# Kernel optimization log

Hardware: AMD Instinct MI355X
Metric: run time of the kernel (lower is better)

Reference implementation:

```python
import jax, jax.numpy as jnp
import numpy as np

B, S, DIM = 32, 1, 4096
N_HEADS, N_KV, HD = 32, 8, 128
N_REP = N_HEADS // N_KV
MAX_SEQ = 2048


def _rope(x, cos, sin):
    # x: [b, s, h, d]; cos/sin: [s, d//2]; rotate consecutive pairs
    x2 = x.reshape(*x.shape[:-1], HD // 2, 2)
    x0, x1 = x2[..., 0], x2[..., 1]
    c = cos[None, :, None, :]
    s = sin[None, :, None, :]
    o0 = x0 * c - x1 * s
    o1 = x0 * s + x1 * c
    return jnp.stack([o0, o1], axis=-1).reshape(x.shape)


def setup_inputs() -> dict:
    key = jax.random.key(0)
    ks = jax.random.split(key, 9)
    start_pos = 2047
    # true RoPE frequencies at position start_pos
    inv_freq = 1.0 / (10000.0 ** (np.arange(0, HD, 2, dtype=np.float32) / HD))
    ang = (start_pos * inv_freq).astype(np.float32)[None, :]  # [1, HD//2]
    return {
        "x": jax.random.normal(ks[0], (B, S, DIM), jnp.float32),
        "freqs_cos": jnp.asarray(np.cos(ang)),
        "freqs_sin": jnp.asarray(np.sin(ang)),
        "wq": jax.random.normal(ks[1], (DIM, DIM), jnp.float32) * 0.02,
        "wk": jax.random.normal(ks[2], (N_KV * HD, DIM), jnp.float32) * 0.02,
        "wv": jax.random.normal(ks[3], (N_KV * HD, DIM), jnp.float32) * 0.02,
        "wo": jax.random.normal(ks[4], (DIM, DIM), jnp.float32) * 0.02,
        "cache_k": jax.random.normal(ks[5], (B, MAX_SEQ, N_KV, HD), jnp.float32),
        "cache_v": jax.random.normal(ks[6], (B, MAX_SEQ, N_KV, HD), jnp.float32),
        "start_pos": start_pos,
    }


def reference(x, freqs_cos, freqs_sin, wq, wk, wv, wo, cache_k, cache_v, start_pos):
    b, s, dim = x.shape  # s == 1 (decode)
    xq = (x @ wq.T).reshape(b, s, N_HEADS, HD)
    xk = (x @ wk.T).reshape(b, s, N_KV, HD)
    xv = (x @ wv.T).reshape(b, s, N_KV, HD)
    xq = _rope(xq, freqs_cos, freqs_sin)
    xk = _rope(xk, freqs_cos, freqs_sin)
    # KV-cache scatter write at start_pos
    cache_k = jax.lax.dynamic_update_slice(cache_k, xk, (0, start_pos, 0, 0))
    cache_v = jax.lax.dynamic_update_slice(cache_v, xv, (0, start_pos, 0, 0))
    t = start_pos + s
    keys = cache_k[:, :t]    # [b, t, kv, hd]
    values = cache_v[:, :t]  # [b, t, kv, hd]
    # GQA: group query heads over kv heads (no repeat_kv materialization)
    q = xq[:, 0].reshape(b, N_KV, N_REP, HD)  # [b, kv, rep, hd]
    scale = HD ** -0.5
    attn = jnp.einsum("bkrd,btkd->bkrt", q, keys) * scale  # [b, kv, rep, t]
    attn = jax.nn.softmax(attn.astype(jnp.float32), axis=-1).astype(q.dtype)
    out = jnp.einsum("bkrt,btkd->bkrd", attn, values).reshape(b, s, dim)
    return out @ wo.T
```

## Files before the change

### kernel.cpp

```cpp
#include <hip/hip_runtime.h>
#include <math.h>

#define B_ 32
#define DIM_ 4096
#define NKV_ 8
#define HD_ 128
#define T_ 2048
#define KS_ 16
#define QKV_ROWS_ 6144
#define O_ROWS_ 4096

#define Q_OFF    0
#define KNEW_OFF (Q_OFF + B_*DIM_)
#define VNEW_OFF (KNEW_OFF + B_*NKV_*HD_)
#define AO_OFF   (VNEW_OFF + B_*NKV_*HD_)
#define PQKV_OFF (AO_OFF + B_*DIM_)
#define PO_OFF   (PQKV_OFF + KS_*QKV_ROWS_*B_)

__device__ __forceinline__ void fma4(float4& a, const float4& x, float w) {
    a.x = fmaf(x.x, w, a.x); a.y = fmaf(x.y, w, a.y);
    a.z = fmaf(x.z, w, a.z); a.w = fmaf(x.w, w, a.w);
}

template<int NROWS>
__global__ __launch_bounds__(256) void gemm_split(
    const float* __restrict__ X, const float* __restrict__ W0,
    const float* __restrict__ W1, const float* __restrict__ W2,
    float* __restrict__ part)
{
    __shared__ float xs[32][36];
    __shared__ float wsh[32][132];
    const int rb = blockIdx.x, ks = blockIdx.y;
    const int row0 = rb * 128;
    const float* W; int wr0;
    if (NROWS == 4096 || row0 < 4096) { W = W0; wr0 = row0; }
    else if (row0 < 5120)             { W = W1; wr0 = row0 - 4096; }
    else                              { W = W2; wr0 = row0 - 5120; }
    const int tid = threadIdx.x;
    const int rt = tid & 31, bt = tid >> 5;
    float4 acc[4];
    acc[0] = acc[1] = acc[2] = acc[3] = make_float4(0.f,0.f,0.f,0.f);
    const int kc0 = ks * 256;
    const int xb = tid >> 3, xkq = tid & 7;
    for (int kt = 0; kt < 8; ++kt) {
        const int kc = kc0 + kt * 32;
        __syncthreads();
        {
            float4 v = *(const float4*)(X + xb * DIM_ + kc + xkq * 4);
            xs[xkq*4+0][xb] = v.x; xs[xkq*4+1][xb] = v.y;
            xs[xkq*4+2][xb] = v.z; xs[xkq*4+3][xb] = v.w;
        }
        #pragma unroll
        for (int j = 0; j < 4; ++j) {
            int f = tid + 256 * j;
            int r = f >> 3, kq = f & 7;
            float4 v = *(const float4*)(W + (wr0 + r) * DIM_ + kc + kq * 4);
            wsh[kq*4+0][r] = v.x; wsh[kq*4+1][r] = v.y;
            wsh[kq*4+2][r] = v.z; wsh[kq*4+3][r] = v.w;
        }
        __syncthreads();
        #pragma unroll
        for (int k = 0; k < 32; ++k) {
            float4 xv = *(const float4*)&xs[k][bt*4];
            float4 wv = *(const float4*)&wsh[k][rt*4];
            fma4(acc[0], xv, wv.x);
            fma4(acc[1], xv, wv.y);
            fma4(acc[2], xv, wv.z);
            fma4(acc[3], xv, wv.w);
        }
    }
    #pragma unroll
    for (int j = 0; j < 4; ++j) {
        const int row = row0 + rt * 4 + j;
        *(float4*)(part + (ks * NROWS + row) * 32 + bt * 4) = acc[j];
    }
}

__global__ __launch_bounds__(256) void reduce_rope(
    const float* __restrict__ part, const float* __restrict__ fc,
    const float* __restrict__ fs, float* __restrict__ qout,
    float* __restrict__ kout, float* __restrict__ vout)
{
    const int t = blockIdx.x * 256 + threadIdx.x;
    const int b = t & 31;
    const int row0 = (t >> 5) * 2;
    float s0 = 0.f, s1 = 0.f;
    #pragma unroll
    for (int ks = 0; ks < KS_; ++ks) {
        const float* p = part + (ks * QKV_ROWS_ + row0) * 32 + b;
        s0 += p[0];
        s1 += p[32];
    }
    if (row0 < 5120) {
        const int i = (row0 & 127) >> 1;
        const float c = fc[i], s = fs[i];
        const float o0 = s0 * c - s1 * s;
        const float o1 = s0 * s + s1 * c;
        if (row0 < 4096) {
            qout[b * 4096 + row0]     = o0;
            qout[b * 4096 + row0 + 1] = o1;
        } else {
            const int lr = row0 - 4096;
            kout[b * 1024 + lr]     = o0;
            kout[b * 1024 + lr + 1] = o1;
        }
    } else {
        const int lr = row0 - 5120;
        vout[b * 1024 + lr]     = s0;
        vout[b * 1024 + lr + 1] = s1;
    }
}

__global__ __launch_bounds__(512) void attn_decode(
    const float* __restrict__ q, const float* __restrict__ knew,
    const float* __restrict__ vnew, const float* __restrict__ ck,
    const float* __restrict__ cv, float* __restrict__ ao)
{
    __shared__ float sc[4 * 2052];
    __shared__ float red[16];
    __shared__ float red3[2048];
    const int b  = blockIdx.x >> 3;
    const int kv = blockIdx.x & 7;
    const int tid = threadIdx.x;
    const int w  = tid >> 6;
    const int ln = tid & 63;
    const int r  = ln >> 4;
    const int ds = ln & 15;
    const float scale = 0.08838834764831845f;

    const float* qp = q + b * 4096 + (kv * 4 + r) * 128 + ds * 8;
    const float4 qa = *(const float4*)qp;
    const float4 qb = *(const float4*)(qp + 4);
    const float* ckb = ck + ((b * 2048) * 8 + kv) * 128;
    const float* knb = knew + (b * 8 + kv) * 128 + ds * 8;

    for (int i = 0; i < 32; ++i) {
        const int tbase = w + 64 * i;
        float4 ka[8], kb[8];
        #pragma unroll
        for (int u = 0; u < 8; ++u) {
            const int t = tbase + 8 * u;
            const float* kp = (t == 2047) ? knb : (ckb + t * 1024 + ds * 8);
            ka[u] = *(const float4*)kp;
            kb[u] = *(const float4*)(kp + 4);
        }
        #pragma unroll
        for (int u = 0; u < 8; ++u) {
            const int t = tbase + 8 * u;
            float d = ka[u].x*qa.x + ka[u].y*qa.y + ka[u].z*qa.z + ka[u].w*qa.w
                    + kb[u].x*qb.x + kb[u].y*qb.y + kb[u].z*qb.z + kb[u].w*qb.w;
            d += __shfl_xor(d, 1);
            d += __shfl_xor(d, 2);
            d += __shfl_xor(d, 4);
            d += __shfl_xor(d, 8);
            if (ds == 0) sc[r * 2052 + t] = d * scale;
        }
    }
    __syncthreads();

    const int m128 = tid & 127;
    const int r2 = tid >> 7;
    float mloc = -1e30f;
    #pragma unroll
    for (int j = 0; j < 16; ++j)
        mloc = fmaxf(mloc, sc[r2 * 2052 + m128 + j * 128]);
    #pragma unroll
    for (int o = 1; o < 64; o <<= 1)
        mloc = fmaxf(mloc, __shfl_xor(mloc, o));
    if (ln == 0) red[w] = mloc;
    __syncthreads();
    const float m = fmaxf(red[r2 * 2], red[r2 * 2 + 1]);
    float sloc = 0.f;
    #pragma unroll
    for (int j = 0; j < 16; ++j) {
        const int idx = r2 * 2052 + m128 + j * 128;
        const float p = __expf(sc[idx] - m);
        sc[idx] = p;
        sloc += p;
    }
    #pragma unroll
    for (int o = 1; o < 64; o <<= 1)
        sloc += __shfl_xor(sloc, o);
    if (ln == 0) red[8 + w] = sloc;
    __syncthreads();

    const int tp = tid >> 7;
    const int r3 = (tid >> 5) & 3;
    const int dq = tid & 31;
    const float* cvb = cv + ((b * 2048) * 8 + kv) * 128 + dq * 4;
    const float* vnb = vnew + (b * 8 + kv) * 128 + dq * 4;
    float4 acc[4];
    acc[0] = acc[1] = acc[2] = acc[3] = make_float4(0.f,0.f,0.f,0.f);
    for (int j = 0; j < 512; j += 4) {
        #pragma unroll
        for (int u = 0; u < 4; ++u) {
            const int t = tp + 4 * (j + u);
            const float* vp = (t == 2047) ? vnb : (cvb + t * 1024);
            const float4 v = *(const float4*)vp;
            const float p = sc[r3 * 2052 + t];
            fma4(acc[u], v, p);
        }
    }
    float4 asum;
    asum.x = (acc[0].x + acc[1].x) + (acc[2].x + acc[3].x);
    asum.y = (acc[0].y + acc[1].y) + (acc[2].y + acc[3].y);
    asum.z = (acc[0].z + acc[1].z) + (acc[2].z + acc[3].z);
    asum.w = (acc[0].w + acc[1].w) + (acc[2].w + acc[3].w);
    *(float4*)&red3[((tp * 4 + r3) * 32 + dq) * 4] = asum;
    __syncthreads();
    if (tid < 128) {
        const int rr = tid >> 5, dqq = tid & 31;
        float4 s = make_float4(0.f,0.f,0.f,0.f);
        #pragma unroll
        for (int t4 = 0; t4 < 4; ++t4) {
            const float4 v = *(const float4*)&red3[((t4 * 4 + rr) * 32 + dqq) * 4];
            s.x += v.x; s.y += v.y; s.z += v.z; s.w += v.w;
        }
        const float invl = 1.f / (red[8 + rr * 2] + red[8 + rr * 2 + 1]);
        s.x *= invl; s.y *= invl; s.z *= invl; s.w *= invl;
        *(float4*)(ao + b * 4096 + (kv * 4 + rr) * 128 + dqq * 4) = s;
    }
}

__global__ __launch_bounds__(256) void reduce_out(
    const float* __restrict__ part, float* __restrict__ out)
{
    const int t = blockIdx.x * 256 + threadIdx.x;
    const int b = t & 31, row = t >> 5;
    float s = 0.f;
    #pragma unroll
    for (int ks = 0; ks < KS_; ++ks)
        s += part[(ks * O_ROWS_ + row) * 32 + b];
    out[b * 4096 + row] = s;
}

extern "C" void kernel_launch(void* const* d_in, const int* in_sizes, int n_in,
                              void* d_out, int out_size, void* d_ws, size_t ws_size,
                              hipStream_t stream)
{
    const float* x  = (const float*)d_in[0];
    const float* fc = (const float*)d_in[1];
    const float* fs = (const float*)d_in[2];
    const float* wq = (const float*)d_in[3];
    const float* wk = (const float*)d_in[4];
    const float* wv = (const float*)d_in[5];
    const float* wo = (const float*)d_in[6];
    const float* ck = (const float*)d_in[7];
    const float* cv = (const float*)d_in[8];
    float* ws   = (float*)d_ws;
    float* q    = ws + Q_OFF;
    float* knew = ws + KNEW_OFF;
    float* vnew = ws + VNEW_OFF;
    float* ao   = ws + AO_OFF;
    float* pqkv = ws + PQKV_OFF;
    float* po   = ws + PO_OFF;

    gemm_split<QKV_ROWS_><<<dim3(48, 16), 256, 0, stream>>>(x, wq, wk, wv, pqkv);
    reduce_rope<<<384, 256, 0, stream>>>(pqkv, fc, fs, q, knew, vnew);
    attn_decode<<<256, 512, 0, stream>>>(q, knew, vnew, ck, cv, ao);
    gemm_split<O_ROWS_><<<dim3(32, 16), 256, 0, stream>>>(ao, wo, wo, wo, po);
    reduce_out<<<512, 256, 0, stream>>>(po, (float*)d_out);
}
```

Baseline: 647.1 us.

## Split decode attention over sequence chunks with flash-decoding merge kernel

Replaces the single attention kernel (256 blocks, one per batch and KV head) with a split-K variant that gives each block a 512-token chunk, for 1024 blocks. Each block also reuses one K load across all four query heads of the group. A new merge kernel combines the per-chunk partial outputs using the saved max and sum values. The aim is more parallelism across the GPU to saturate bandwidth on the 128 MB KV cache read, at the cost of an extra launch and some partial-result traffic.

```diff
diff --git a/kernel.cpp b/kernel.cpp
--- a/kernel.cpp
+++ b/kernel.cpp
@@ -9,6 +9,7 @@
 #define KS_ 16
 #define QKV_ROWS_ 6144
 #define O_ROWS_ 4096
+#define NSPLIT_ 4
 
 #define Q_OFF    0
 #define KNEW_OFF (Q_OFF + B_*DIM_)
@@ -16,6 +17,8 @@
 #define AO_OFF   (VNEW_OFF + B_*NKV_*HD_)
 #define PQKV_OFF (AO_OFF + B_*DIM_)
 #define PO_OFF   (PQKV_OFF + KS_*QKV_ROWS_*B_)
+#define OPART_OFF (PO_OFF + KS_*O_ROWS_*B_)
+#define ML_OFF   (OPART_OFF + B_*NKV_*NSPLIT_*4*HD_)
 
 __device__ __forceinline__ void fma4(float4& a, const float4& x, float w) {
     a.x = fmaf(x.x, w, a.x); a.y = fmaf(x.y, w, a.y);
@@ -111,115 +114,168 @@
     }
 }
 
-__global__ __launch_bounds__(512) void attn_decode(
+__global__ __launch_bounds__(256, 4) void attn_split(
     const float* __restrict__ q, const float* __restrict__ knew,
     const float* __restrict__ vnew, const float* __restrict__ ck,
-    const float* __restrict__ cv, float* __restrict__ ao)
-{
-    __shared__ float sc[4 * 2052];
-    __shared__ float red[16];
-    __shared__ float red3[2048];
-    const int b  = blockIdx.x >> 3;
-    const int kv = blockIdx.x & 7;
+    const float* __restrict__ cv, float* __restrict__ opart,
+    float* __restrict__ ml)
+{
+    __shared__ float sct[512 * 4];
+    __shared__ float red[2048];
+    const int sp = blockIdx.x & 3;
+    const int kv = (blockIdx.x >> 2) & 7;
+    const int b  = blockIdx.x >> 5;
     const int tid = threadIdx.x;
     const int w  = tid >> 6;
     const int ln = tid & 63;
-    const int r  = ln >> 4;
-    const int ds = ln & 15;
+    const int t0 = sp * 512;
     const float scale = 0.08838834764831845f;
 
-    const float* qp = q + b * 4096 + (kv * 4 + r) * 128 + ds * 8;
-    const float4 qa = *(const float4*)qp;
-    const float4 qb = *(const float4*)(qp + 4);
-    const float* ckb = ck + ((b * 2048) * 8 + kv) * 128;
-    const float* knb = knew + (b * 8 + kv) * 128 + ds * 8;
-
-    for (int i = 0; i < 32; ++i) {
-        const int tbase = w + 64 * i;
-        float4 ka[8], kb[8];
+    const int tl = ln >> 4, dsl = ln & 15;
+    float4 qr[4][2];
+    #pragma unroll
+    for (int r = 0; r < 4; ++r) {
+        const float* qp = q + b * 4096 + (kv * 4 + r) * 128 + dsl * 8;
+        qr[r][0] = *(const float4*)qp;
+        qr[r][1] = *(const float4*)(qp + 4);
+    }
+    const float* ckb = ck + ((size_t)(b * 2048) * 8 + kv) * 128;
+    const float* knb = knew + (b * 8 + kv) * 128 + dsl * 8;
+
+    for (int tt = 0; tt < 32; tt += 4) {
+        float4 ka[4][2];
+        int ri[4];
+        #pragma unroll
+        for (int u = 0; u < 4; ++u) {
+            ri[u] = w * 128 + (tt + u) * 4 + tl;
+            const int gt = t0 + ri[u];
+            const float* kp = (gt == 2047) ? knb
+                              : (ckb + (size_t)gt * 1024 + dsl * 8);
+            ka[u][0] = *(const float4*)kp;
+            ka[u][1] = *(const float4*)(kp + 4);
+        }
+        #pragma unroll
+        for (int u = 0; u < 4; ++u) {
+            float d[4];
+            #pragma unroll
+            for (int r = 0; r < 4; ++r) {
+                float t1 = ka[u][0].x*qr[r][0].x + ka[u][0].y*qr[r][0].y
+                         + ka[u][0].z*qr[r][0].z + ka[u][0].w*qr[r][0].w;
+                float t2 = ka[u][1].x*qr[r][1].x + ka[u][1].y*qr[r][1].y
+                         + ka[u][1].z*qr[r][1].z + ka[u][1].w*qr[r][1].w;
+                float dd = t1 + t2;
+                dd += __shfl_xor(dd, 1);
+                dd += __shfl_xor(dd, 2);
+                dd += __shfl_xor(dd, 4);
+                dd += __shfl_xor(dd, 8);
+                d[r] = dd * scale;
+            }
+            if (dsl == 0)
+                *(float4*)&sct[ri[u] * 4] = make_float4(d[0], d[1], d[2], d[3]);
+        }
+    }
+    __syncthreads();
+
+    float vals[8];
+    #pragma unroll
+    for (int j = 0; j < 8; ++j)
+        vals[j] = sct[(j * 64 + ln) * 4 + w];
+    float m = vals[0];
+    #pragma unroll
+    for (int j = 1; j < 8; ++j) m = fmaxf(m, vals[j]);
+    #pragma unroll
+    for (int o = 1; o < 64; o <<= 1)
+        m = fmaxf(m, __shfl_xor(m, o));
+    float l = 0.f;
+    #pragma unroll
+    for (int j = 0; j < 8; ++j) {
+        const float p = __expf(vals[j] - m);
+        sct[(j * 64 + ln) * 4 + w] = p;
+        l += p;
+    }
+    #pragma unroll
+    for (int o = 1; o < 64; o <<= 1)
+        l += __shfl_xor(l, o);
+    if (ln == 0) {
+        const int idx = ((b * 8 + kv) * 4 + sp) * 8 + w * 2;
+        ml[idx]     = m;
+        ml[idx + 1] = l;
+    }
+    __syncthreads();
+
+    float2 acc[4];
+    #pragma unroll
+    for (int r = 0; r < 4; ++r) acc[r] = make_float2(0.f, 0.f);
+    const float* cvb = cv + ((size_t)(b * 2048) * 8 + kv) * 128 + ln * 2;
+    const float* vnb = vnew + (b * 8 + kv) * 128 + ln * 2;
+    for (int j = 0; j < 128; j += 8) {
+        float2 vv[8];
         #pragma unroll
         for (int u = 0; u < 8; ++u) {
-            const int t = tbase + 8 * u;
-            const float* kp = (t == 2047) ? knb : (ckb + t * 1024 + ds * 8);
-            ka[u] = *(const float4*)kp;
-            kb[u] = *(const float4*)(kp + 4);
+            const int gt = t0 + w * 128 + j + u;
+            const float* vp = (gt == 2047) ? vnb : (cvb + (size_t)gt * 1024);
+            vv[u] = *(const float2*)vp;
         }
         #pragma unroll
         for (int u = 0; u < 8; ++u) {
-            const int t = tbase + 8 * u;
-            float d = ka[u].x*qa.x + ka[u].y*qa.y + ka[u].z*qa.z + ka[u].w*qa.w
-                    + kb[u].x*qb.x + kb[u].y*qb.y + kb[u].z*qb.z + kb[u].w*qb.w;
-            d += __shfl_xor(d, 1);
-            d += __shfl_xor(d, 2);
-            d += __shfl_xor(d, 4);
-            d += __shfl_xor(d, 8);
-            if (ds == 0) sc[r * 2052 + t] = d * scale;
-        }
-    }
+            const int ri = w * 128 + j + u;
+            const float4 p4 = *(const float4*)&sct[ri * 4];
+            acc[0].x = fmaf(vv[u].x, p4.x, acc[0].x);
+            acc[0].y = fmaf(vv[u].y, p4.x, acc[0].y);
+            acc[1].x = fmaf(vv[u].x, p4.y, acc[1].x);
+            acc[1].y = fmaf(vv[u].y, p4.y, acc[1].y);
+            acc[2].x = fmaf(vv[u].x, p4.z, acc[2].x);
+            acc[2].y = fmaf(vv[u].y, p4.z, acc[2].y);
+            acc[3].x = fmaf(vv[u].x, p4.w, acc[3].x);
+            acc[3].y = fmaf(vv[u].y, p4.w, acc[3].y);
+        }
+    }
+    #pragma unroll
+    for (int r = 0; r < 4; ++r)
+        *(float2*)&red[((w * 4 + r) * 64 + ln) * 2] = acc[r];
     __syncthreads();
-
-    const int m128 = tid & 127;
-    const int r2 = tid >> 7;
-    float mloc = -1e30f;
-    #pragma unroll
-    for (int j = 0; j < 16; ++j)
-        mloc = fmaxf(mloc, sc[r2 * 2052 + m128 + j * 128]);
-    #pragma unroll
-    for (int o = 1; o < 64; o <<= 1)
-        mloc = fmaxf(mloc, __shfl_xor(mloc, o));
-    if (ln == 0) red[w] = mloc;
-    __syncthreads();
-    const float m = fmaxf(red[r2 * 2], red[r2 * 2 + 1]);
-    float sloc = 0.f;
-    #pragma unroll
-    for (int j = 0; j < 16; ++j) {
-        const int idx = r2 * 2052 + m128 + j * 128;
-        const float p = __expf(sc[idx] - m);
-        sc[idx] = p;
-        sloc += p;
-    }
-    #pragma unroll
-    for (int o = 1; o < 64; o <<= 1)
-        sloc += __shfl_xor(sloc, o);
-    if (ln == 0) red[8 + w] = sloc;
-    __syncthreads();
-
-    const int tp = tid >> 7;
-    const int r3 = (tid >> 5) & 3;
-    const int dq = tid & 31;
-    const float* cvb = cv + ((b * 2048) * 8 + kv) * 128 + dq * 4;
-    const float* vnb = vnew + (b * 8 + kv) * 128 + dq * 4;
-    float4 acc[4];
-    acc[0] = acc[1] = acc[2] = acc[3] = make_float4(0.f,0.f,0.f,0.f);
-    for (int j = 0; j < 512; j += 4) {
-        #pragma unroll
-        for (int u = 0; u < 4; ++u) {
-            const int t = tp + 4 * (j + u);
-            const float* vp = (t == 2047) ? vnb : (cvb + t * 1024);
-            const float4 v = *(const float4*)vp;
-            const float p = sc[r3 * 2052 + t];
-            fma4(acc[u], v, p);
-        }
-    }
-    float4 asum;
-    asum.x = (acc[0].x + acc[1].x) + (acc[2].x + acc[3].x);
-    asum.y = (acc[0].y + acc[1].y) + (acc[2].y + acc[3].y);
-    asum.z = (acc[0].z + acc[1].z) + (acc[2].z + acc[3].z);
-    asum.w = (acc[0].w + acc[1].w) + (acc[2].w + acc[3].w);
-    *(float4*)&red3[((tp * 4 + r3) * 32 + dq) * 4] = asum;
-    __syncthreads();
-    if (tid < 128) {
-        const int rr = tid >> 5, dqq = tid & 31;
-        float4 s = make_float4(0.f,0.f,0.f,0.f);
-        #pragma unroll
-        for (int t4 = 0; t4 < 4; ++t4) {
-            const float4 v = *(const float4*)&red3[((t4 * 4 + rr) * 32 + dqq) * 4];
-            s.x += v.x; s.y += v.y; s.z += v.z; s.w += v.w;
-        }
-        const float invl = 1.f / (red[8 + rr * 2] + red[8 + rr * 2 + 1]);
-        s.x *= invl; s.y *= invl; s.z *= invl; s.w *= invl;
-        *(float4*)(ao + b * 4096 + (kv * 4 + rr) * 128 + dqq * 4) = s;
-    }
+    {
+        const int r = tid >> 6, dd = tid & 63;
+        float2 s = make_float2(0.f, 0.f);
+        #pragma unroll
+        for (int ww = 0; ww < 4; ++ww) {
+            const float2 v = *(const float2*)&red[((ww * 4 + r) * 64 + dd) * 2];
+            s.x += v.x; s.y += v.y;
+        }
+        const int ob = (((b * 8 + kv) * 4 + sp) * 4 + r) * 128 + dd * 2;
+        *(float2*)&opart[ob] = s;
+    }
+}
+
+__global__ __launch_bounds__(128) void attn_merge(
+    const float* __restrict__ opart, const float* __restrict__ ml,
+    float* __restrict__ ao)
+{
+    const int bk = blockIdx.x;
+    const int tid = threadIdx.x;
+    const int r = tid >> 5, dq = tid & 31;
+    float m[4], l[4];
+    #pragma unroll
+    for (int sp = 0; sp < 4; ++sp) {
+        m[sp] = ml[(bk * 4 + sp) * 8 + r * 2];
+        l[sp] = ml[(bk * 4 + sp) * 8 + r * 2 + 1];
+    }
+    const float M = fmaxf(fmaxf(m[0], m[1]), fmaxf(m[2], m[3]));
+    float wgt[4], L = 0.f;
+    #pragma unroll
+    for (int sp = 0; sp < 4; ++sp) {
+        wgt[sp] = __expf(m[sp] - M);
+        L += l[sp] * wgt[sp];
+    }
+    float4 o = make_float4(0.f, 0.f, 0.f, 0.f);
+    #pragma unroll
+    for (int sp = 0; sp < 4; ++sp) {
+        const float4 v = *(const float4*)&opart[((bk * 4 + sp) * 4 + r) * 128 + dq * 4];
+        fma4(o, v, wgt[sp]);
+    }
+    const float inv = 1.f / L;
+    o.x *= inv; o.y *= inv; o.z *= inv; o.w *= inv;
+    *(float4*)&ao[bk * 512 + r * 128 + dq * 4] = o;
 }
 
 __global__ __launch_bounds__(256) void reduce_out(
@@ -247,17 +303,20 @@
     const float* wo = (const float*)d_in[6];
     const float* ck = (const float*)d_in[7];
     const float* cv = (const float*)d_in[8];
-    float* ws   = (float*)d_ws;
-    float* q    = ws + Q_OFF;
-    float* knew = ws + KNEW_OFF;
-    float* vnew = ws + VNEW_OFF;
-    float* ao   = ws + AO_OFF;
-    float* pqkv = ws + PQKV_OFF;
-    float* po   = ws + PO_OFF;
+    float* ws    = (float*)d_ws;
+    float* q     = ws + Q_OFF;
+    float* knew  = ws + KNEW_OFF;
+    float* vnew  = ws + VNEW_OFF;
+    float* ao    = ws + AO_OFF;
+    float* pqkv  = ws + PQKV_OFF;
+    float* po    = ws + PO_OFF;
+    float* opart = ws + OPART_OFF;
+    float* mlp   = ws + ML_OFF;
 
     gemm_split<QKV_ROWS_><<<dim3(48, 16), 256, 0, stream>>>(x, wq, wk, wv, pqkv);
     reduce_rope<<<384, 256, 0, stream>>>(pqkv, fc, fs, q, knew, vnew);
-    attn_decode<<<256, 512, 0, stream>>>(q, knew, vnew, ck, cv, ao);
+    attn_split<<<1024, 256, 0, stream>>>(q, knew, vnew, ck, cv, opart, mlp);
+    attn_merge<<<256, 128, 0, stream>>>(opart, mlp, ao);
     gemm_split<O_ROWS_><<<dim3(32, 16), 256, 0, stream>>>(ao, wo, wo, wo, po);
     reduce_out<<<512, 256, 0, stream>>>(po, (float*)d_out);
 }
```

Measured after the change: 646.6 us. No clear change (-0.1%).
